# Optimization experiments

Measured on AMD Instinct MI355X. Metric: run time of the kernel, lower is better.

## Reference

```python
import jax, jax.numpy as jnp
from jax import lax
import numpy as np

# Geometry fixed by __init__ (see shape_source)
UP = 2          # up_factor[0]
DOWN = 2        # down_factor[0]
PAD_LO = 11
PAD_HI = 10
SLOPE = 0.2
GAIN = np.sqrt(2.0).astype(np.float32)


def _kaiser_beta(atten):
    if atten > 50:
        return 0.1102 * (atten - 8.7)
    if atten > 21:
        return 0.5842 * (atten - 21.0) ** 0.4 + 0.07886 * (atten - 21.0)
    return 0.0


def _firwin(numtaps, cutoff, width, fs):
    # numpy re-implementation of scipy.signal.firwin(numtaps, cutoff, width=width, fs=fs)
    nyq = fs / 2.0
    atten = 2.285 * (numtaps - 1) * np.pi * (width / nyq) + 7.95  # kaiser_atten
    beta = _kaiser_beta(atten)
    m = np.arange(numtaps) - (numtaps - 1) / 2.0
    fc = cutoff / nyq
    h = fc * np.sinc(fc * m) * np.kaiser(numtaps, beta)
    h = h / h.sum()  # unity DC gain (pass_zero scaling)
    return h.astype(np.float32)


def _depthwise_conv1d(x, f, axis, stride=1, lhs_dilation=1, padding=(0, 0)):
    """Depthwise 1D FIR along spatial `axis` (2 or 3) of NCHW tensor.
    Filter is flipped (true convolution, as in upfirdn2d)."""
    C = x.shape[1]
    k = f.shape[0]
    fr = f[::-1]
    if axis == 2:
        kern = jnp.broadcast_to(fr.reshape(1, 1, k, 1), (C, 1, k, 1))
        strides, ld, pads = (stride, 1), (lhs_dilation, 1), [padding, (0, 0)]
    else:
        kern = jnp.broadcast_to(fr.reshape(1, 1, 1, k), (C, 1, 1, k))
        strides, ld, pads = (1, stride), (1, lhs_dilation), [(0, 0), padding]
    return lax.conv_general_dilated(
        x, kern, window_strides=strides, padding=pads, lhs_dilation=ld,
        dimension_numbers=('NCHW', 'OIHW', 'NCHW'), feature_group_count=C)


def setup_inputs() -> dict:
    key = jax.random.key(0)
    k1, k2 = jax.random.split(key)
    x = jax.random.normal(k1, (32, 128, 64, 64), dtype=jnp.float32)
    bias = jax.random.normal(k2, (128,), dtype=jnp.float32) * 0.1
    # up filter: numtaps=12, cutoff=in_cutoff=28, width=2*in_half_width=8, fs=tmp_sr=128
    up_filter = jnp.asarray(_firwin(12, 28.0, 8.0, 128.0))
    # down filter: numtaps=12, cutoff=out_cutoff=28, width=2*out_half_width=8, fs=128
    down_filter = jnp.asarray(_firwin(12, 28.0, 8.0, 128.0))
    return {"x": x, "bias": bias, "up_filter": up_filter, "down_filter": down_filter}


def reference(x, bias, up_filter, down_filter):
    # filtered_lrelu reference: upfirdn2d(up, fu, gain=up**2) -> bias -> lrelu*sqrt(2) -> upfirdn2d(down, fd)
    # Zero-insertion upsampling fused via lhs_dilation; dilated length is H*UP-(UP-1),
    # so the trailing UP-1 zeros of the nominal H*UP upsampled signal move into pad_hi.
    fu = up_filter * UP  # gain up per separable pass -> up**2 total
    pad = (PAD_LO, PAD_HI + UP - 1)
    y = _depthwise_conv1d(x, fu, axis=2, lhs_dilation=UP, padding=pad)
    y = _depthwise_conv1d(y, fu, axis=3, lhs_dilation=UP, padding=pad)  # [B,C,138,138]
    y = y + bias[None, :, None, None]
    y = jnp.where(y >= 0, y, SLOPE * y) * GAIN
    y = _depthwise_conv1d(y, down_filter, axis=2, stride=DOWN)
    y = _depthwise_conv1d(y, down_filter, axis=3, stride=DOWN)  # [B,C,64,64]
    return y
```

## Files before the change

kernel.cpp:

```cpp
#include <hip/hip_runtime.h>


#define NT 512
#define GAIN 1.41421356237309504880f
#define C1 (0.6f * GAIN)
#define C2 (0.4f * GAIN)

#define ZROWS 42
#define ZSTRIDE 84
#define ZPAD 8
#define YSTRIDE 148
#define YWSTRIDE 68

#define ZB_OFF 0
#define YB_OFF (ZROWS * ZSTRIDE)
#define YW_OFF 0
#define LDS_FLOATS (YB_OFF + ZROWS * YSTRIDE)

__device__ __forceinline__ float sload(float v) {
    return __uint_as_float(__builtin_amdgcn_readfirstlane(__float_as_uint(v)));
}

__global__ __launch_bounds__(NT, 8) void fused_upfirdn_lrelu(
    const float* __restrict__ x,
    const float* __restrict__ bias,
    const float* __restrict__ upf,
    const float* __restrict__ dnf,
    float* __restrict__ out)
{
    extern __shared__ float lds[];
    float* zb = lds + ZB_OFF;
    float* yb = lds + YB_OFF;
    float* yw = lds + YW_OFF;

    const int t = threadIdx.x;
    const int bid = blockIdx.x;
    const int s = bid >> 2;
    const int o0 = (bid & 3) << 4;
    const int c = s & 127;

    float fu[12], fd[12];
#pragma unroll
    for (int j = 0; j < 12; ++j) {
        fu[j] = sload(2.0f * upf[j]);
        fd[j] = sload(dnf[j]);
    }
    const float bv = sload(bias[c]);

    const float* xg = x + (size_t)s * 4096;
    float* outg = out + (size_t)s * 4096;

    if (t < 336) {
        const int m = t >> 4;
        const int c4 = (t & 15) << 2;
        const int M = o0 + m;
        float4 xv[6];
        if (M >= 5 && M <= 63) {
#pragma unroll
            for (int d = 0; d < 6; ++d)
                xv[d] = *reinterpret_cast<const float4*>(xg + (M - 5 + d) * 64 + c4);
        } else {
#pragma unroll
            for (int d = 0; d < 6; ++d) {
                const int r = M - 5 + d;
                xv[d] = (r >= 0 && r <= 63)
                      ? *reinterpret_cast<const float4*>(xg + r * 64 + c4)
                      : make_float4(0.f, 0.f, 0.f, 0.f);
            }
        }
        float a0[4] = {0,0,0,0}, a1[4] = {0,0,0,0};
#pragma unroll
        for (int d = 0; d < 6; ++d) {
            const float w0 = fu[2 * (5 - d)], w1 = fu[2 * (5 - d) + 1];
            a0[0] += w0 * xv[d].x; a0[1] += w0 * xv[d].y; a0[2] += w0 * xv[d].z; a0[3] += w0 * xv[d].w;
            a1[0] += w1 * xv[d].x; a1[1] += w1 * xv[d].y; a1[2] += w1 * xv[d].z; a1[3] += w1 * xv[d].w;
        }
        float* zr = zb + (2 * m) * ZSTRIDE + ZPAD + c4;
        *reinterpret_cast<float4*>(zr)           = make_float4(a0[0], a0[1], a0[2], a0[3]);
        *reinterpret_cast<float4*>(zr + ZSTRIDE) = make_float4(a1[0], a1[1], a1[2], a1[3]);
    } else {
        for (int pt = t - 336; pt < 210; pt += 176) {
            const int rl = pt / 5;
            const int p = pt - rl * 5;
            const int col = (p < 2) ? (p << 2) : (72 + ((p - 2) << 2));
            *reinterpret_cast<float4*>(zb + rl * ZSTRIDE + col) = make_float4(0.f, 0.f, 0.f, 0.f);
        }
    }
    __syncthreads();

    if (t < 432) {
        const int cg = t / 48;
        const int il = t - cg * 48;
        if (il < ZROWS) {
            const int mbase = cg << 3;
            const float* zr = zb + il * ZSTRIDE + mbase;
            float zv[16];
#pragma unroll
            for (int q = 0; q < 4; ++q) {
                const float4 v = *reinterpret_cast<const float4*>(zr + (q << 2));
                zv[4 * q] = v.x; zv[4 * q + 1] = v.y; zv[4 * q + 2] = v.z; zv[4 * q + 3] = v.w;
            }
            float yv[16];
#pragma unroll
            for (int e = 0; e < 8; ++e) {
                float a0 = bv, a1 = bv;
#pragma unroll
                for (int tt = 0; tt < 6; ++tt) {
                    const float zz = zv[8 + e - tt];
                    a0 += fu[2 * tt]     * zz;
                    a1 += fu[2 * tt + 1] * zz;
                }
                yv[2 * e]     = C1 * a0 + C2 * fabsf(a0);
                yv[2 * e + 1] = C1 * a1 + C2 * fabsf(a1);
            }
            float* yr = yb + il * YSTRIDE + (mbase << 1);
#pragma unroll
            for (int q = 0; q < 4; ++q)
                *reinterpret_cast<float4*>(yr + (q << 2)) =
                    make_float4(yv[4 * q], yv[4 * q + 1], yv[4 * q + 2], yv[4 * q + 3]);
        }
    }
    __syncthreads();

    if (t < 384) {
        const int cg = t / 48;
        const int il = t - cg * 48;
        if (il < ZROWS) {
            const float* yr = yb + il * YSTRIDE + (cg << 4);
            float w[28];
#pragma unroll
            for (int q = 0; q < 7; ++q) {
                const float4 v = *reinterpret_cast<const float4*>(yr + (q << 2));
                w[4 * q] = v.x; w[4 * q + 1] = v.y; w[4 * q + 2] = v.z; w[4 * q + 3] = v.w;
            }
            float rv[8];
#pragma unroll
            for (int e = 0; e < 8; ++e) {
                float a = 0.0f;
#pragma unroll
                for (int j = 0; j < 12; ++j) a += fd[j] * w[2 * e + 11 - j];
                rv[e] = a;
            }
            float* wr = yw + il * YWSTRIDE + (cg << 3);
            *reinterpret_cast<float4*>(wr)     = make_float4(rv[0], rv[1], rv[2], rv[3]);
            *reinterpret_cast<float4*>(wr + 4) = make_float4(rv[4], rv[5], rv[6], rv[7]);
        }
    }
    __syncthreads();

    if (t < 64) {
        const int eg = t >> 4;
        const int col4 = (t & 15) << 2;
        const float* wr = yw + (eg << 3) * YWSTRIDE + col4;
        float acc[4][4] = {{0,0,0,0},{0,0,0,0},{0,0,0,0},{0,0,0,0}};
#pragma unroll
        for (int r = 0; r < 18; ++r) {
            const float4 v = *reinterpret_cast<const float4*>(wr + r * YWSTRIDE);
#pragma unroll
            for (int e = 0; e < 4; ++e) {
                if (r >= 2 * e && r <= 2 * e + 11) {
                    const float ww = fd[11 - r + 2 * e];
                    acc[e][0] += ww * v.x; acc[e][1] += ww * v.y;
                    acc[e][2] += ww * v.z; acc[e][3] += ww * v.w;
                }
            }
        }
#pragma unroll
        for (int e = 0; e < 4; ++e)
            *reinterpret_cast<float4*>(outg + (o0 + (eg << 2) + e) * 64 + col4) =
                make_float4(acc[e][0], acc[e][1], acc[e][2], acc[e][3]);
    }
}

extern "C" void kernel_launch(void* const* d_in, const int* in_sizes, int n_in,
                              void* d_out, int out_size, void* d_ws, size_t ws_size,
                              hipStream_t stream) {
    const float* x    = (const float*)d_in[0];
    const float* bias = (const float*)d_in[1];
    const float* upf  = (const float*)d_in[2];
    const float* dnf  = (const float*)d_in[3];
    float* out = (float*)d_out;

    const int n_blocks = 32 * 128 * 4;
    const size_t lds_bytes = (size_t)LDS_FLOATS * sizeof(float);
    hipLaunchKernelGGL(fused_upfirdn_lrelu, dim3(n_blocks), dim3(NT),
                       lds_bytes, stream, x, bias, upf, dnf, out);
}
```

Measured before the change: 74.97 us.

## Fuse horizontal upsample+lrelu stage into horizontal downsample stage in registers

Merges the horizontal up-FIR, bias, and leaky-ReLU stage with the horizontal down-FIR stage. Each thread now recomputes the 26 upsampled values it needs directly from z in registers instead of reading them from an intermediate LDS buffer. This removes one LDS round trip, one barrier, and the yb buffer, which cuts LDS use and may raise occupancy. The cost is extra redundant up-FIR arithmetic on halo columns and higher register pressure from the 24-element window plus accumulators.

```diff
diff --git a/kernel.cpp b/kernel.cpp
--- a/kernel.cpp
+++ b/kernel.cpp
@@ -9,13 +9,11 @@
 #define ZROWS 42
 #define ZSTRIDE 84
 #define ZPAD 8
-#define YSTRIDE 148
 #define YWSTRIDE 68
 
 #define ZB_OFF 0
-#define YB_OFF (ZROWS * ZSTRIDE)
-#define YW_OFF 0
-#define LDS_FLOATS (YB_OFF + ZROWS * YSTRIDE)
+#define YW_OFF (ZROWS * ZSTRIDE)
+#define LDS_FLOATS (YW_OFF + ZROWS * YWSTRIDE)
 
 __device__ __forceinline__ float sload(float v) {
     return __uint_as_float(__builtin_amdgcn_readfirstlane(__float_as_uint(v)));
@@ -30,7 +28,6 @@
 {
     extern __shared__ float lds[];
     float* zb = lds + ZB_OFF;
-    float* yb = lds + YB_OFF;
     float* yw = lds + YW_OFF;
 
     const int t = threadIdx.x;
@@ -88,62 +85,40 @@
     }
     __syncthreads();
 
-    if (t < 432) {
-        const int cg = t / 48;
-        const int il = t - cg * 48;
-        if (il < ZROWS) {
-            const int mbase = cg << 3;
-            const float* zr = zb + il * ZSTRIDE + mbase;
-            float zv[16];
-#pragma unroll
-            for (int q = 0; q < 4; ++q) {
-                const float4 v = *reinterpret_cast<const float4*>(zr + (q << 2));
-                zv[4 * q] = v.x; zv[4 * q + 1] = v.y; zv[4 * q + 2] = v.z; zv[4 * q + 3] = v.w;
-            }
-            float yv[16];
-#pragma unroll
-            for (int e = 0; e < 8; ++e) {
-                float a0 = bv, a1 = bv;
-#pragma unroll
-                for (int tt = 0; tt < 6; ++tt) {
-                    const float zz = zv[8 + e - tt];
-                    a0 += fu[2 * tt]     * zz;
-                    a1 += fu[2 * tt + 1] * zz;
-                }
-                yv[2 * e]     = C1 * a0 + C2 * fabsf(a0);
-                yv[2 * e + 1] = C1 * a1 + C2 * fabsf(a1);
-            }
-            float* yr = yb + il * YSTRIDE + (mbase << 1);
-#pragma unroll
-            for (int q = 0; q < 4; ++q)
-                *reinterpret_cast<float4*>(yr + (q << 2)) =
-                    make_float4(yv[4 * q], yv[4 * q + 1], yv[4 * q + 2], yv[4 * q + 3]);
-        }
-    }
-    __syncthreads();
-
     if (t < 384) {
         const int cg = t / 48;
         const int il = t - cg * 48;
         if (il < ZROWS) {
-            const float* yr = yb + il * YSTRIDE + (cg << 4);
-            float w[28];
+            const float* zr = zb + il * ZSTRIDE + (cg << 3);
+            float zv[24];
 #pragma unroll
-            for (int q = 0; q < 7; ++q) {
-                const float4 v = *reinterpret_cast<const float4*>(yr + (q << 2));
-                w[4 * q] = v.x; w[4 * q + 1] = v.y; w[4 * q + 2] = v.z; w[4 * q + 3] = v.w;
+            for (int q = 0; q < 6; ++q) {
+                const float4 v = *reinterpret_cast<const float4*>(zr + (q << 2));
+                zv[4 * q] = v.x; zv[4 * q + 1] = v.y; zv[4 * q + 2] = v.z; zv[4 * q + 3] = v.w;
             }
-            float rv[8];
+            float acc[8] = {0, 0, 0, 0, 0, 0, 0, 0};
 #pragma unroll
-            for (int e = 0; e < 8; ++e) {
-                float a = 0.0f;
+            for (int v = 0; v < 13; ++v) {
+                float a0 = bv, a1 = bv;
 #pragma unroll
-                for (int j = 0; j < 12; ++j) a += fd[j] * w[2 * e + 11 - j];
-                rv[e] = a;
+                for (int tt = 0; tt < 6; ++tt) {
+                    const float zz = zv[v + 8 - tt];
+                    a0 += fu[2 * tt]     * zz;
+                    a1 += fu[2 * tt + 1] * zz;
+                }
+                const float y0 = C1 * a0 + C2 * fabsf(a0);
+                const float y1 = C1 * a1 + C2 * fabsf(a1);
+#pragma unroll
+                for (int e = 0; e < 8; ++e) {
+                    const int j0 = 2 * e + 11 - 2 * v;
+                    const int j1 = 2 * e + 10 - 2 * v;
+                    if (j0 >= 0 && j0 <= 11) acc[e] += fd[j0] * y0;
+                    if (j1 >= 0 && j1 <= 11) acc[e] += fd[j1] * y1;
+                }
             }
             float* wr = yw + il * YWSTRIDE + (cg << 3);
-            *reinterpret_cast<float4*>(wr)     = make_float4(rv[0], rv[1], rv[2], rv[3]);
-            *reinterpret_cast<float4*>(wr + 4) = make_float4(rv[4], rv[5], rv[6], rv[7]);
+            *reinterpret_cast<float4*>(wr)     = make_float4(acc[0], acc[1], acc[2], acc[3]);
+            *reinterpret_cast<float4*>(wr + 4) = make_float4(acc[4], acc[5], acc[6], acc[7]);
         }
     }
     __syncthreads();
```

Result: slower. 83.26 us (+11.1%).

## Process two output strips per block and prefetch second strip's input during first

Applied to the files above, without the earlier changes.

Each block now handles two 16-row output strips in sequence instead of one, which halves the grid size. The global loads for the second strip are issued before the first strip's final vertical downsampling pass, with a scheduling barrier, so load latency can overlap with LDS compute. This amortizes block launch and filter/bias setup costs. In exchange it adds more serial barriers per block, keeps the prefetched registers live for longer (raising register pressure), and gives less parallelism across the grid.

```diff
diff --git a/kernel.cpp b/kernel.cpp
--- a/kernel.cpp
+++ b/kernel.cpp
@@ -19,6 +19,136 @@
 
 __device__ __forceinline__ float sload(float v) {
     return __uint_as_float(__builtin_amdgcn_readfirstlane(__float_as_uint(v)));
+}
+
+__device__ __forceinline__ void load6(float4* xv, const float* __restrict__ xg,
+                                      int M, int c4) {
+    if (M >= 5 && M <= 63) {
+#pragma unroll
+        for (int d = 0; d < 6; ++d)
+            xv[d] = *reinterpret_cast<const float4*>(xg + (M - 5 + d) * 64 + c4);
+    } else {
+#pragma unroll
+        for (int d = 0; d < 6; ++d) {
+            const int r = M - 5 + d;
+            xv[d] = (r >= 0 && r <= 63)
+                  ? *reinterpret_cast<const float4*>(xg + r * 64 + c4)
+                  : make_float4(0.f, 0.f, 0.f, 0.f);
+        }
+    }
+}
+
+__device__ __forceinline__ void uph(const float4* xv, const float* fu,
+                                    float* a0, float* a1) {
+#pragma unroll
+    for (int k = 0; k < 4; ++k) { a0[k] = 0.f; a1[k] = 0.f; }
+#pragma unroll
+    for (int d = 0; d < 6; ++d) {
+        const float w0 = fu[2 * (5 - d)], w1 = fu[2 * (5 - d) + 1];
+        a0[0] += w0 * xv[d].x; a0[1] += w0 * xv[d].y; a0[2] += w0 * xv[d].z; a0[3] += w0 * xv[d].w;
+        a1[0] += w1 * xv[d].x; a1[1] += w1 * xv[d].y; a1[2] += w1 * xv[d].z; a1[3] += w1 * xv[d].w;
+    }
+}
+
+__device__ __forceinline__ void zwrite(float* zb, int m, int c4,
+                                       const float* a0, const float* a1) {
+    float* zr = zb + (2 * m) * ZSTRIDE + ZPAD + c4;
+    *reinterpret_cast<float4*>(zr)           = make_float4(a0[0], a0[1], a0[2], a0[3]);
+    *reinterpret_cast<float4*>(zr + ZSTRIDE) = make_float4(a1[0], a1[1], a1[2], a1[3]);
+}
+
+__device__ __forceinline__ void padzero(float* zb, int t) {
+    for (int pt = t - 336; pt < 210; pt += 176) {
+        const int rl = pt / 5;
+        const int p = pt - rl * 5;
+        const int col = (p < 2) ? (p << 2) : (72 + ((p - 2) << 2));
+        *reinterpret_cast<float4*>(zb + rl * ZSTRIDE + col) = make_float4(0.f, 0.f, 0.f, 0.f);
+    }
+}
+
+__device__ __forceinline__ void p2(const float* zb, float* yb, int t,
+                                   const float* fu, float bv) {
+    if (t >= 432) return;
+    const int cg = t / 48;
+    const int il = t - cg * 48;
+    if (il >= ZROWS) return;
+    const int mbase = cg << 3;
+    const float* zr = zb + il * ZSTRIDE + mbase;
+    float zv[16];
+#pragma unroll
+    for (int q = 0; q < 4; ++q) {
+        const float4 v = *reinterpret_cast<const float4*>(zr + (q << 2));
+        zv[4 * q] = v.x; zv[4 * q + 1] = v.y; zv[4 * q + 2] = v.z; zv[4 * q + 3] = v.w;
+    }
+    float yv[16];
+#pragma unroll
+    for (int e = 0; e < 8; ++e) {
+        float a0 = bv, a1 = bv;
+#pragma unroll
+        for (int tt = 0; tt < 6; ++tt) {
+            const float zz = zv[8 + e - tt];
+            a0 += fu[2 * tt]     * zz;
+            a1 += fu[2 * tt + 1] * zz;
+        }
+        yv[2 * e]     = C1 * a0 + C2 * fabsf(a0);
+        yv[2 * e + 1] = C1 * a1 + C2 * fabsf(a1);
+    }
+    float* yr = yb + il * YSTRIDE + (mbase << 1);
+#pragma unroll
+    for (int q = 0; q < 4; ++q)
+        *reinterpret_cast<float4*>(yr + (q << 2)) =
+            make_float4(yv[4 * q], yv[4 * q + 1], yv[4 * q + 2], yv[4 * q + 3]);
+}
+
+__device__ __forceinline__ void p3(const float* yb, float* yw, int t,
+                                   const float* fd) {
+    if (t >= 384) return;
+    const int cg = t / 48;
+    const int il = t - cg * 48;
+    if (il >= ZROWS) return;
+    const float* yr = yb + il * YSTRIDE + (cg << 4);
+    float w[28];
+#pragma unroll
+    for (int q = 0; q < 7; ++q) {
+        const float4 v = *reinterpret_cast<const float4*>(yr + (q << 2));
+        w[4 * q] = v.x; w[4 * q + 1] = v.y; w[4 * q + 2] = v.z; w[4 * q + 3] = v.w;
+    }
+    float rv[8];
+#pragma unroll
+    for (int e = 0; e < 8; ++e) {
+        float a = 0.0f;
+#pragma unroll
+        for (int j = 0; j < 12; ++j) a += fd[j] * w[2 * e + 11 - j];
+        rv[e] = a;
+    }
+    float* wr = yw + il * YWSTRIDE + (cg << 3);
+    *reinterpret_cast<float4*>(wr)     = make_float4(rv[0], rv[1], rv[2], rv[3]);
+    *reinterpret_cast<float4*>(wr + 4) = make_float4(rv[4], rv[5], rv[6], rv[7]);
+}
+
+__device__ __forceinline__ void p4(const float* yw, float* __restrict__ outg,
+                                   int o0, int t, const float* fd) {
+    if (t >= 64) return;
+    const int eg = t >> 4;
+    const int col4 = (t & 15) << 2;
+    const float* wr = yw + (eg << 3) * YWSTRIDE + col4;
+    float acc[4][4] = {{0,0,0,0},{0,0,0,0},{0,0,0,0},{0,0,0,0}};
+#pragma unroll
+    for (int r = 0; r < 18; ++r) {
+        const float4 v = *reinterpret_cast<const float4*>(wr + r * YWSTRIDE);
+#pragma unroll
+        for (int e = 0; e < 4; ++e) {
+            if (r >= 2 * e && r <= 2 * e + 11) {
+                const float ww = fd[11 - r + 2 * e];
+                acc[e][0] += ww * v.x; acc[e][1] += ww * v.y;
+                acc[e][2] += ww * v.z; acc[e][3] += ww * v.w;
+            }
+        }
+    }
+#pragma unroll
+    for (int e = 0; e < 4; ++e)
+        *reinterpret_cast<float4*>(outg + (o0 + (eg << 2) + e) * 64 + col4) =
+            make_float4(acc[e][0], acc[e][1], acc[e][2], acc[e][3]);
 }
 
 __global__ __launch_bounds__(NT, 8) void fused_upfirdn_lrelu(
@@ -35,8 +165,10 @@
 
     const int t = threadIdx.x;
     const int bid = blockIdx.x;
-    const int s = bid >> 2;
-    const int o0 = (bid & 3) << 4;
+    const int s = bid >> 1;
+    const int h = bid & 1;
+    const int o0A = h << 5;
+    const int o0B = o0A + 16;
     const int c = s & 127;
 
     float fu[12], fd[12];
@@ -50,126 +182,49 @@
     const float* xg = x + (size_t)s * 4096;
     float* outg = out + (size_t)s * 4096;
 
+    const int p1_m  = t >> 4;
+    const int p1_c4 = (t & 15) << 2;
+
+    float4 sx[6];
+
     if (t < 336) {
-        const int m = t >> 4;
-        const int c4 = (t & 15) << 2;
-        const int M = o0 + m;
-        float4 xv[6];
-        if (M >= 5 && M <= 63) {
-#pragma unroll
-            for (int d = 0; d < 6; ++d)
-                xv[d] = *reinterpret_cast<const float4*>(xg + (M - 5 + d) * 64 + c4);
-        } else {
-#pragma unroll
-            for (int d = 0; d < 6; ++d) {
-                const int r = M - 5 + d;
-                xv[d] = (r >= 0 && r <= 63)
-                      ? *reinterpret_cast<const float4*>(xg + r * 64 + c4)
-                      : make_float4(0.f, 0.f, 0.f, 0.f);
-            }
-        }
-        float a0[4] = {0,0,0,0}, a1[4] = {0,0,0,0};
-#pragma unroll
-        for (int d = 0; d < 6; ++d) {
-            const float w0 = fu[2 * (5 - d)], w1 = fu[2 * (5 - d) + 1];
-            a0[0] += w0 * xv[d].x; a0[1] += w0 * xv[d].y; a0[2] += w0 * xv[d].z; a0[3] += w0 * xv[d].w;
-            a1[0] += w1 * xv[d].x; a1[1] += w1 * xv[d].y; a1[2] += w1 * xv[d].z; a1[3] += w1 * xv[d].w;
-        }
-        float* zr = zb + (2 * m) * ZSTRIDE + ZPAD + c4;
-        *reinterpret_cast<float4*>(zr)           = make_float4(a0[0], a0[1], a0[2], a0[3]);
-        *reinterpret_cast<float4*>(zr + ZSTRIDE) = make_float4(a1[0], a1[1], a1[2], a1[3]);
+        load6(sx, xg, o0A + p1_m, p1_c4);
+        float a0[4], a1[4];
+        uph(sx, fu, a0, a1);
+        zwrite(zb, p1_m, p1_c4, a0, a1);
     } else {
-        for (int pt = t - 336; pt < 210; pt += 176) {
-            const int rl = pt / 5;
-            const int p = pt - rl * 5;
-            const int col = (p < 2) ? (p << 2) : (72 + ((p - 2) << 2));
-            *reinterpret_cast<float4*>(zb + rl * ZSTRIDE + col) = make_float4(0.f, 0.f, 0.f, 0.f);
-        }
-    }
-    __syncthreads();
-
-    if (t < 432) {
-        const int cg = t / 48;
-        const int il = t - cg * 48;
-        if (il < ZROWS) {
-            const int mbase = cg << 3;
-            const float* zr = zb + il * ZSTRIDE + mbase;
-            float zv[16];
-#pragma unroll
-            for (int q = 0; q < 4; ++q) {
-                const float4 v = *reinterpret_cast<const float4*>(zr + (q << 2));
-                zv[4 * q] = v.x; zv[4 * q + 1] = v.y; zv[4 * q + 2] = v.z; zv[4 * q + 3] = v.w;
-            }
-            float yv[16];
-#pragma unroll
-            for (int e = 0; e < 8; ++e) {
-                float a0 = bv, a1 = bv;
-#pragma unroll
-                for (int tt = 0; tt < 6; ++tt) {
-                    const float zz = zv[8 + e - tt];
-                    a0 += fu[2 * tt]     * zz;
-                    a1 += fu[2 * tt + 1] * zz;
-                }
-                yv[2 * e]     = C1 * a0 + C2 * fabsf(a0);
-                yv[2 * e + 1] = C1 * a1 + C2 * fabsf(a1);
-            }
-            float* yr = yb + il * YSTRIDE + (mbase << 1);
-#pragma unroll
-            for (int q = 0; q < 4; ++q)
-                *reinterpret_cast<float4*>(yr + (q << 2)) =
-                    make_float4(yv[4 * q], yv[4 * q + 1], yv[4 * q + 2], yv[4 * q + 3]);
-        }
-    }
-    __syncthreads();
-
-    if (t < 384) {
-        const int cg = t / 48;
-        const int il = t - cg * 48;
-        if (il < ZROWS) {
-            const float* yr = yb + il * YSTRIDE + (cg << 4);
-            float w[28];
-#pragma unroll
-            for (int q = 0; q < 7; ++q) {
-                const float4 v = *reinterpret_cast<const float4*>(yr + (q << 2));
-                w[4 * q] = v.x; w[4 * q + 1] = v.y; w[4 * q + 2] = v.z; w[4 * q + 3] = v.w;
-            }
-            float rv[8];
-#pragma unroll
-            for (int e = 0; e < 8; ++e) {
-                float a = 0.0f;
-#pragma unroll
-                for (int j = 0; j < 12; ++j) a += fd[j] * w[2 * e + 11 - j];
-                rv[e] = a;
-            }
-            float* wr = yw + il * YWSTRIDE + (cg << 3);
-            *reinterpret_cast<float4*>(wr)     = make_float4(rv[0], rv[1], rv[2], rv[3]);
-            *reinterpret_cast<float4*>(wr + 4) = make_float4(rv[4], rv[5], rv[6], rv[7]);
-        }
-    }
-    __syncthreads();
-
-    if (t < 64) {
-        const int eg = t >> 4;
-        const int col4 = (t & 15) << 2;
-        const float* wr = yw + (eg << 3) * YWSTRIDE + col4;
-        float acc[4][4] = {{0,0,0,0},{0,0,0,0},{0,0,0,0},{0,0,0,0}};
-#pragma unroll
-        for (int r = 0; r < 18; ++r) {
-            const float4 v = *reinterpret_cast<const float4*>(wr + r * YWSTRIDE);
-#pragma unroll
-            for (int e = 0; e < 4; ++e) {
-                if (r >= 2 * e && r <= 2 * e + 11) {
-                    const float ww = fd[11 - r + 2 * e];
-                    acc[e][0] += ww * v.x; acc[e][1] += ww * v.y;
-                    acc[e][2] += ww * v.z; acc[e][3] += ww * v.w;
-                }
-            }
-        }
-#pragma unroll
-        for (int e = 0; e < 4; ++e)
-            *reinterpret_cast<float4*>(outg + (o0 + (eg << 2) + e) * 64 + col4) =
-                make_float4(acc[e][0], acc[e][1], acc[e][2], acc[e][3]);
-    }
+        padzero(zb, t);
+    }
+    __syncthreads();
+
+    p2(zb, yb, t, fu, bv);
+    __syncthreads();
+
+    p3(yb, yw, t, fd);
+    __syncthreads();
+
+    if (t < 336) load6(sx, xg, o0B + p1_m, p1_c4);
+    __builtin_amdgcn_sched_barrier(0);
+
+    p4(yw, outg, o0A, t, fd);
+    __syncthreads();
+
+    if (t < 336) {
+        float a0[4], a1[4];
+        uph(sx, fu, a0, a1);
+        zwrite(zb, p1_m, p1_c4, a0, a1);
+    } else {
+        padzero(zb, t);
+    }
+    __syncthreads();
+
+    p2(zb, yb, t, fu, bv);
+    __syncthreads();
+
+    p3(yb, yw, t, fd);
+    __syncthreads();
+
+    p4(yw, outg, o0B, t, fd);
 }
 
 extern "C" void kernel_launch(void* const* d_in, const int* in_sizes, int n_in,
@@ -181,7 +236,7 @@
     const float* dnf  = (const float*)d_in[3];
     float* out = (float*)d_out;
 
-    const int n_blocks = 32 * 128 * 4;
+    const int n_blocks = 32 * 128 * 2;
     const size_t lds_bytes = (size_t)LDS_FLOATS * sizeof(float);
     hipLaunchKernelGGL(fused_upfirdn_lrelu, dim3(n_blocks), dim3(NT),
                        lds_bytes, stream, x, bias, upf, dnf, out);
```

Result: slower. 116.6 us (+55.6%).

## Store intermediate activations as packed bf16 in LDS and shrink block to 384 threads

Applied to the files above, without the earlier changes.

The post-lrelu intermediate is now packed into bf16 pairs with v_cvt_pk_bf16_f32, which halves its LDS footprint and read traffic. The block drops from 512 to 384 threads, and the horizontal-up stage gains a second pass so all 432 work items are still covered. A smaller LDS allocation and fewer threads per block should raise occupancy. The cost is bf16 rounding of the intermediate, which adds precision error that may exceed tolerance.

```diff
diff --git a/kernel.cpp b/kernel.cpp
--- a/kernel.cpp
+++ b/kernel.cpp
@@ -1,7 +1,7 @@
 #include <hip/hip_runtime.h>
 
 
-#define NT 512
+#define NT 384
 #define GAIN 1.41421356237309504880f
 #define C1 (0.6f * GAIN)
 #define C2 (0.4f * GAIN)
@@ -9,16 +9,22 @@
 #define ZROWS 42
 #define ZSTRIDE 84
 #define ZPAD 8
-#define YSTRIDE 148
+#define YSTRIDE_U32 76
 #define YWSTRIDE 68
 
 #define ZB_OFF 0
 #define YB_OFF (ZROWS * ZSTRIDE)
 #define YW_OFF 0
-#define LDS_FLOATS (YB_OFF + ZROWS * YSTRIDE)
+#define LDS_WORDS (YB_OFF + ZROWS * YSTRIDE_U32)
 
 __device__ __forceinline__ float sload(float v) {
     return __uint_as_float(__builtin_amdgcn_readfirstlane(__float_as_uint(v)));
+}
+
+__device__ __forceinline__ unsigned int pk_bf16(float a, float b) {
+    unsigned int r;
+    asm("v_cvt_pk_bf16_f32 %0, %1, %2" : "=v"(r) : "v"(a), "v"(b));
+    return r;
 }
 
 __global__ __launch_bounds__(NT, 8) void fused_upfirdn_lrelu(
@@ -30,7 +36,7 @@
 {
     extern __shared__ float lds[];
     float* zb = lds + ZB_OFF;
-    float* yb = lds + YB_OFF;
+    unsigned int* yb = reinterpret_cast<unsigned int*>(lds + YB_OFF);
     float* yw = lds + YW_OFF;
 
     const int t = threadIdx.x;
@@ -79,7 +85,7 @@
         *reinterpret_cast<float4*>(zr)           = make_float4(a0[0], a0[1], a0[2], a0[3]);
         *reinterpret_cast<float4*>(zr + ZSTRIDE) = make_float4(a1[0], a1[1], a1[2], a1[3]);
     } else {
-        for (int pt = t - 336; pt < 210; pt += 176) {
+        for (int pt = t - 336; pt < 210; pt += 48) {
             const int rl = pt / 5;
             const int p = pt - rl * 5;
             const int col = (p < 2) ? (p << 2) : (72 + ((p - 2) << 2));
@@ -88,9 +94,12 @@
     }
     __syncthreads();
 
-    if (t < 432) {
-        const int cg = t / 48;
-        const int il = t - cg * 48;
+#pragma unroll
+    for (int pass = 0; pass < 2; ++pass) {
+        const int tt = t + pass * NT;
+        if (pass == 1 && t >= 48) break;
+        const int cg = tt / 48;
+        const int il = tt - cg * 48;
         if (il < ZROWS) {
             const int mbase = cg << 3;
             const float* zr = zb + il * ZSTRIDE + mbase;
@@ -100,38 +109,43 @@
                 const float4 v = *reinterpret_cast<const float4*>(zr + (q << 2));
                 zv[4 * q] = v.x; zv[4 * q + 1] = v.y; zv[4 * q + 2] = v.z; zv[4 * q + 3] = v.w;
             }
-            float yv[16];
+            unsigned int pk[8];
 #pragma unroll
             for (int e = 0; e < 8; ++e) {
                 float a0 = bv, a1 = bv;
 #pragma unroll
-                for (int tt = 0; tt < 6; ++tt) {
-                    const float zz = zv[8 + e - tt];
-                    a0 += fu[2 * tt]     * zz;
-                    a1 += fu[2 * tt + 1] * zz;
+                for (int tq = 0; tq < 6; ++tq) {
+                    const float zz = zv[8 + e - tq];
+                    a0 += fu[2 * tq]     * zz;
+                    a1 += fu[2 * tq + 1] * zz;
                 }
-                yv[2 * e]     = C1 * a0 + C2 * fabsf(a0);
-                yv[2 * e + 1] = C1 * a1 + C2 * fabsf(a1);
-            }
-            float* yr = yb + il * YSTRIDE + (mbase << 1);
-#pragma unroll
-            for (int q = 0; q < 4; ++q)
-                *reinterpret_cast<float4*>(yr + (q << 2)) =
-                    make_float4(yv[4 * q], yv[4 * q + 1], yv[4 * q + 2], yv[4 * q + 3]);
+                const float y0 = C1 * a0 + C2 * fabsf(a0);
+                const float y1 = C1 * a1 + C2 * fabsf(a1);
+                pk[e] = pk_bf16(y0, y1);
+            }
+            unsigned int* yr = yb + il * YSTRIDE_U32 + mbase;
+            *reinterpret_cast<uint4*>(yr)     = make_uint4(pk[0], pk[1], pk[2], pk[3]);
+            *reinterpret_cast<uint4*>(yr + 4) = make_uint4(pk[4], pk[5], pk[6], pk[7]);
         }
     }
     __syncthreads();
 
-    if (t < 384) {
+    {
         const int cg = t / 48;
         const int il = t - cg * 48;
         if (il < ZROWS) {
-            const float* yr = yb + il * YSTRIDE + (cg << 4);
-            float w[28];
-#pragma unroll
-            for (int q = 0; q < 7; ++q) {
-                const float4 v = *reinterpret_cast<const float4*>(yr + (q << 2));
-                w[4 * q] = v.x; w[4 * q + 1] = v.y; w[4 * q + 2] = v.z; w[4 * q + 3] = v.w;
+            const unsigned int* yr = yb + il * YSTRIDE_U32 + (cg << 3);
+            unsigned int u[16];
+#pragma unroll
+            for (int q = 0; q < 4; ++q) {
+                const uint4 v = *reinterpret_cast<const uint4*>(yr + (q << 2));
+                u[4 * q] = v.x; u[4 * q + 1] = v.y; u[4 * q + 2] = v.z; u[4 * q + 3] = v.w;
+            }
+            float w[26];
+#pragma unroll
+            for (int k = 0; k < 13; ++k) {
+                w[2 * k]     = __uint_as_float(u[k] << 16);
+                w[2 * k + 1] = __uint_as_float(u[k] & 0xffff0000u);
             }
             float rv[8];
 #pragma unroll
@@ -182,7 +196,7 @@
     float* out = (float*)d_out;
 
     const int n_blocks = 32 * 128 * 4;
-    const size_t lds_bytes = (size_t)LDS_FLOATS * sizeof(float);
+    const size_t lds_bytes = (size_t)LDS_WORDS * sizeof(float);
     hipLaunchKernelGGL(fused_upfirdn_lrelu, dim3(n_blocks), dim3(NT),
                        lds_bytes, stream, x, bias, upf, dnf, out);
 }
```

Result: slower. 79.66 us (+6.3%).
